# Optimization experiments

Hardware: AMD Instinct MI355X
Metric: run time of the kernel (lower is better)

Reference implementation:

```python
import jax, jax.numpy as jnp
import numpy as np

N0, N1, N2 = 100000, 300000, 150000
P = 2
DIM = 64


def spmm(rows, cols, vals, dense, n_rows):
    # sparse[n_rows, n_cols] @ dense[n_cols, d] via gather + segment_sum
    return jax.ops.segment_sum(vals[:, None] * dense[cols], rows, num_segments=n_rows)


def powcat(X, p):
    # torch.cat([X**1, ..., X**p], dim=1)
    return jnp.concatenate([X ** n for n in range(1, p + 1)], axis=1)


def setup_inputs() -> dict:
    key = jax.random.key(0)
    ks = iter(jax.random.split(key, 64))

    def randn(shape, scale=1.0):
        return jax.random.normal(next(ks), shape, dtype=jnp.float32) * scale

    def sparse(nr, nc, nnz):
        r = jax.random.randint(next(ks), (nnz,), 0, nr, dtype=jnp.int32)
        c = jax.random.randint(next(ks), (nnz,), 0, nc, dtype=jnp.int32)
        v = randn((nnz,), 0.1)
        return r, c, v

    inp = {}
    inp["X0"] = randn((N0, DIM))
    inp["X1"] = randn((N1, DIM))
    inp["X2"] = randn((N2, DIM))
    for name, nr, nc, nnz in [
        ("L0", N0, N0, 1000000),
        ("L1", N1, N1, 2400000),
        ("L2", N2, N2, 1200000),
        ("D1invB1", N0, N1, 600000),
        ("D2B1TD1inv", N1, N0, 600000),
        ("B2TD2inv", N2, N1, 450000),
        ("B2D3", N1, N2, 450000),
    ]:
        r, c, v = sparse(nr, nc, nnz)
        inp[name + "_rows"], inp[name + "_cols"], inp[name + "_vals"] = r, c, v
    wscale = 1.0 / np.sqrt(DIM * P)
    for name in ["n2n", "n2e", "e2e", "e2n", "e2t", "t2e", "t2t"]:
        inp["W_" + name] = randn((DIM * P, DIM), wscale)
        inp["b_" + name] = randn((DIM,), wscale)
    return inp


def reference(X0, X1, X2,
              L0_rows, L0_cols, L0_vals,
              L1_rows, L1_cols, L1_vals,
              L2_rows, L2_cols, L2_vals,
              D1invB1_rows, D1invB1_cols, D1invB1_vals,
              D2B1TD1inv_rows, D2B1TD1inv_cols, D2B1TD1inv_vals,
              B2TD2inv_rows, B2TD2inv_cols, B2TD2inv_vals,
              B2D3_rows, B2D3_cols, B2D3_vals,
              W_n2n, b_n2n, W_n2e, b_n2e, W_e2e, b_e2e, W_e2n, b_e2n,
              W_e2t, b_e2t, W_t2e, b_t2e, W_t2t, b_t2t):
    X0c = powcat(X0, P)  # [N0, 2*d]
    X1c = powcat(X1, P)  # [N1, 2*d]
    X2c = powcat(X2, P)  # [N2, 2*d]

    n2n = spmm(L0_rows, L0_cols, L0_vals, X0c @ W_n2n + b_n2n, N0)
    n2e = spmm(D2B1TD1inv_rows, D2B1TD1inv_cols, D2B1TD1inv_vals, X0c @ W_n2e + b_n2e, N1)
    e2n = spmm(D1invB1_rows, D1invB1_cols, D1invB1_vals, X1c @ W_e2n + b_e2n, N0)
    e2e = spmm(L1_rows, L1_cols, L1_vals, X1c @ W_e2e + b_e2e, N1)
    e2t = spmm(B2TD2inv_rows, B2TD2inv_cols, B2TD2inv_vals, X1c @ W_e2t + b_e2t, N2)
    t2t = spmm(L2_rows, L2_cols, L2_vals, X2c @ W_t2t + b_t2t, N2)
    t2e = spmm(B2D3_rows, B2D3_cols, B2D3_vals, X2c @ W_t2e + b_t2e, N1)

    Y0 = 0.5 * jax.nn.relu(n2n + e2n)
    Y1 = (1.0 / 3.0) * jax.nn.relu(e2e + n2e + t2e)
    Y2 = 0.5 * jax.nn.relu(t2t + e2t)
    return (Y0, Y1, Y2)
```

## Files before the change

### kernel.cpp

```cpp
#include <hip/hip_runtime.h>
#include <hip/hip_bf16.h>


#define RPB 128
#define CAP 2048
#define COL_MASK 0x7FFFFu
#define LROW_SH 19
#define DID_SH 26
#define MAXNB 4352
#define MAXNG 544
#define GRID_BIN 512

typedef __attribute__((ext_vector_type(8))) short short8;
typedef __attribute__((ext_vector_type(4))) float f32x4;

__device__ __forceinline__ int   ntld_i(const int* p)   { return __builtin_nontemporal_load(p); }
__device__ __forceinline__ float ntld_f(const float* p) { return __builtin_nontemporal_load(p); }
__device__ __forceinline__ float4 ntld_f4(const float* p) {
    const unsigned long long* q = (const unsigned long long*)p;
    unsigned long long a = __builtin_nontemporal_load(q);
    unsigned long long b = __builtin_nontemporal_load(q + 1);
    float4 v;
    v.x = __uint_as_float((unsigned)a);
    v.y = __uint_as_float((unsigned)(a >> 32));
    v.z = __uint_as_float((unsigned)b);
    v.w = __uint_as_float((unsigned)(b >> 32));
    return v;
}
__device__ __forceinline__ void ntst_f4(float* p, float4 v) {
    unsigned long long a = (unsigned long long)__float_as_uint(v.x)
                         | ((unsigned long long)__float_as_uint(v.y) << 32);
    unsigned long long b = (unsigned long long)__float_as_uint(v.z)
                         | ((unsigned long long)__float_as_uint(v.w) << 32);
    unsigned long long* q = (unsigned long long*)p;
    __builtin_nontemporal_store(a, q);
    __builtin_nontemporal_store(b, q + 1);
}

__device__ __forceinline__ unsigned short f2bf(float f) {
    unsigned u = __float_as_uint(f);
    unsigned r = u + 0x7FFFu + ((u >> 16) & 1u);
    return (unsigned short)(r >> 16);
}

__device__ __forceinline__ void split8(float4 a0, float4 a1, short8& hi, short8& lo) {
    float v[8] = {a0.x, a0.y, a0.z, a0.w, a1.x, a1.y, a1.z, a1.w};
    #pragma unroll
    for (int e = 0; e < 8; ++e) {
        unsigned short h = f2bf(v[e]);
        float hf = __uint_as_float((unsigned)h << 16);
        hi[e] = (short)h;
        lo[e] = (short)f2bf(v[e] - hf);
    }
}

struct WAll { const float* w[7]; };

__global__ __launch_bounds__(256) void winit(WAll wa, unsigned short* __restrict__ frags)
{
    const int s = blockIdx.x;
    const float* __restrict__ W = wa.w[s];
    unsigned short* __restrict__ out = frags + (size_t)s * 16384;
    for (int slot = threadIdx.x; slot < 1024; slot += 256) {
        const int l  = slot & 63;
        const int nf = (slot >> 6) & 3;
        const int kk = slot >> 8;
        const int col = nf * 16 + (l & 15);
        const int kb  = kk * 32 + 8 * (l >> 4);
        short8 vh, vl;
        #pragma unroll
        for (int e = 0; e < 8; ++e) {
            float w = W[(size_t)(kb + e) * 64 + col];
            unsigned short h = f2bf(w);
            float hf = __uint_as_float((unsigned)h << 16);
            vh[e] = (short)h;
            vl[e] = (short)f2bf(w - hf);
        }
        *(short8*)(out + ((size_t)((kk * 4 + nf) * 2 + 0) * 64 + l) * 8) = vh;
        *(short8*)(out + ((size_t)((kk * 4 + nf) * 2 + 1) * 64 + l) * 8) = vl;
    }
}

__device__ __forceinline__ void mfma_set(
    const short8 Ah[4], const short8 Al[4],
    const unsigned short* __restrict__ F, const float* __restrict__ bias,
    unsigned short* __restrict__ D, int nrows, int row0w, int l)
{
    const int lg = l >> 4, lr = l & 15;
    const short8* __restrict__ Fv = (const short8*)F;
    f32x4 acc[4];
    #pragma unroll
    for (int nf = 0; nf < 4; ++nf) {
        float b = bias[nf * 16 + lr];
        f32x4 bi = {b, b, b, b};
        acc[nf] = bi;
    }
    #pragma unroll
    for (int kk = 0; kk < 4; ++kk) {
        #pragma unroll
        for (int nf = 0; nf < 4; ++nf) {
            short8 bh = Fv[((kk * 4 + nf) * 2 + 0) * 64 + l];
            short8 bl = Fv[((kk * 4 + nf) * 2 + 1) * 64 + l];
            acc[nf] = __builtin_amdgcn_mfma_f32_16x16x32_bf16(Ah[kk], bh, acc[nf], 0, 0, 0);
            acc[nf] = __builtin_amdgcn_mfma_f32_16x16x32_bf16(Al[kk], bh, acc[nf], 0, 0, 0);
            acc[nf] = __builtin_amdgcn_mfma_f32_16x16x32_bf16(Ah[kk], bl, acc[nf], 0, 0, 0);
        }
    }
    #pragma unroll
    for (int nf = 0; nf < 4; ++nf) {
        #pragma unroll
        for (int j = 0; j < 4; ++j) {
            int row = row0w + lg * 4 + j;
            if (row < nrows)
                D[(size_t)row * 64 + nf * 16 + lr] = f2bf(acc[nf][j]);
        }
    }
}

__global__ __launch_bounds__(256) void gemm_powcat_mfma(
    const float* __restrict__ X, int nrows, int nsets,
    const unsigned short* __restrict__ F0, const float* __restrict__ b0, unsigned short* __restrict__ D0,
    const unsigned short* __restrict__ F1, const float* __restrict__ b1, unsigned short* __restrict__ D1,
    const unsigned short* __restrict__ F2, const float* __restrict__ b2, unsigned short* __restrict__ D2)
{
    __shared__ float Xs[64][68];
    const int tid = threadIdx.x;
    const int row0 = blockIdx.x * 64;

    #pragma unroll
    for (int it = 0; it < 4; ++it) {
        int idx = tid + it * 256;
        int r = idx >> 4, c4 = idx & 15;
        float4 v = make_float4(0.f, 0.f, 0.f, 0.f);
        if (row0 + r < nrows)
            v = ntld_f4(X + (size_t)(row0 + r) * 64 + c4 * 4);
        *(float4*)&Xs[r][c4 * 4] = v;
    }
    __syncthreads();

    const int w = tid >> 6, l = tid & 63;
    const int lg = l >> 4, lr = l & 15;

    short8 Ah[4], Al[4];
    #pragma unroll
    for (int kk = 0; kk < 4; ++kk) {
        const float* p = &Xs[w * 16 + lr][(kk & 1) * 32 + 8 * lg];
        float4 a0 = *(const float4*)p;
        float4 a1 = *(const float4*)(p + 4);
        if (kk >= 2) {
            a0.x *= a0.x; a0.y *= a0.y; a0.z *= a0.z; a0.w *= a0.w;
            a1.x *= a1.x; a1.y *= a1.y; a1.z *= a1.z; a1.w *= a1.w;
        }
        split8(a0, a1, Ah[kk], Al[kk]);
    }

    const int row0w = row0 + w * 16;
    mfma_set(Ah, Al, F0, b0, D0, nrows, row0w, l);
    if (nsets > 1) mfma_set(Ah, Al, F1, b1, D1, nrows, row0w, l);
    if (nsets > 2) mfma_set(Ah, Al, F2, b2, D2, nrows, row0w, l);
}

struct Bin7 {
    const int *r0, *r1, *r2, *r3, *r4, *r5, *r6;
    const int *c0, *c1, *c2, *c3, *c4, *c5, *c6;
    const float *v0, *v1, *v2, *v3, *v4, *v5, *v6;
    int p1, p2, p3, p4, p5, p6, p7;
    int t0, t1, t2, t3, t4, t5, t6;
};

struct Ent { int r; int tb; unsigned cw; float v; };

template<bool FULL>
__device__ __forceinline__ Ent decode(const Bin7& B, int i) {
    Ent e;
    if (i < B.p1) {
        int li = i;
        e.r = ntld_i(B.r0 + li); e.tb = B.t0;
        if (FULL) { e.cw = (unsigned)ntld_i(B.c0 + li) | (0u << DID_SH); e.v = ntld_f(B.v0 + li); }
    } else if (i < B.p2) {
        int li = i - B.p1;
        e.r = ntld_i(B.r1 + li); e.tb = B.t1;
        if (FULL) { e.cw = (unsigned)ntld_i(B.c1 + li) | (1u << DID_SH); e.v = ntld_f(B.v1 + li); }
    } else if (i < B.p3) {
        int li = i - B.p2;
        e.r = ntld_i(B.r2 + li); e.tb = B.t2;
        if (FULL) { e.cw = (unsigned)ntld_i(B.c2 + li) | (2u << DID_SH); e.v = ntld_f(B.v2 + li); }
    } else if (i < B.p4) {
        int li = i - B.p3;
        e.r = ntld_i(B.r3 + li); e.tb = B.t3;
        if (FULL) { e.cw = (unsigned)ntld_i(B.c3 + li) | (3u << DID_SH); e.v = ntld_f(B.v3 + li); }
    } else if (i < B.p5) {
        int li = i - B.p4;
        e.r = ntld_i(B.r4 + li); e.tb = B.t4;
        if (FULL) { e.cw = (unsigned)ntld_i(B.c4 + li) | (4u << DID_SH); e.v = ntld_f(B.v4 + li); }
    } else if (i < B.p6) {
        int li = i - B.p5;
        e.r = ntld_i(B.r5 + li); e.tb = B.t5;
        if (FULL) { e.cw = (unsigned)ntld_i(B.c5 + li) | (5u << DID_SH); e.v = ntld_f(B.v5 + li); }
    } else {
        int li = i - B.p6;
        e.r = ntld_i(B.r6 + li); e.tb = B.t6;
        if (FULL) { e.cw = (unsigned)ntld_i(B.c6 + li) | (6u << DID_SH); e.v = ntld_f(B.v6 + li); }
    }
    return e;
}

__global__ __launch_bounds__(1024) void bhist_grp(
    Bin7 B, int* __restrict__ gcount, int NG, int chunk)
{
    __shared__ int h[MAXNG];
    for (int i = threadIdx.x; i < NG; i += 1024) h[i] = 0;
    __syncthreads();
    const int s = blockIdx.x * chunk;
    int e = s + chunk;  if (e > B.p7) e = B.p7;
    for (int i = s + threadIdx.x; i < e; i += 1024) {
        Ent en = decode<false>(B, i);
        atomicAdd(&h[(en.tb + (en.r >> 7)) >> 3], 1);
    }
    __syncthreads();
    for (int i = threadIdx.x; i < NG; i += 1024)
        if (h[i]) atomicAdd(&gcount[i], h[i]);
}

__global__ __launch_bounds__(1024) void scatter_grp(
    Bin7 B, int* __restrict__ gcur, uint2* __restrict__ payA,
    int NG, int chunk)
{
    __shared__ int lbase[MAXNG];
    __shared__ int lcur[MAXNG];
    for (int i = threadIdx.x; i < NG; i += 1024) lcur[i] = 0;
    __syncthreads();
    const int s = blockIdx.x * chunk;
    int e = s + chunk;  if (e > B.p7) e = B.p7;

    for (int i = s + threadIdx.x; i < e; i += 1024) {
        Ent en = decode<false>(B, i);
        atomicAdd(&lcur[(en.tb + (en.r >> 7)) >> 3], 1);
    }
    __syncthreads();
    for (int i = threadIdx.x; i < NG; i += 1024) {
        int c = lcur[i];
        lbase[i] = c ? atomicAdd(&gcur[i], c) : 0;
        lcur[i] = 0;
    }
    __syncthreads();
    for (int i = s + threadIdx.x; i < e; i += 1024) {
        Ent en = decode<true>(B, i);
        int b = en.tb + (en.r >> 7);
        int g = b >> 3;
        int pos = lbase[g] + atomicAdd(&lcur[g], 1);
        unsigned col = en.cw & COL_MASK;
        unsigned did = en.cw >> DID_SH;
        unsigned cwA = col | ((unsigned)(en.r & 127) << LROW_SH)
                     | ((unsigned)(b & 7) << 26) | (did << 29);
        payA[pos] = make_uint2(cwA, __float_as_uint(en.v));
    }
}

__global__ __launch_bounds__(1024) void sort_grp(
    const uint2* __restrict__ payA, const int* __restrict__ goff,
    const int* __restrict__ gcur, int* __restrict__ boff,
    int* __restrict__ bend, uint2* __restrict__ payB, int NBtot)
{
    __shared__ int cnt[8], cur[8];
    const int g = blockIdx.x;
    const int b0 = g * 8;
    const int seg0 = goff[g], seg1 = gcur[g];
    if (threadIdx.x < 8) cnt[threadIdx.x] = 0;
    __syncthreads();
    for (int i = seg0 + threadIdx.x; i < seg1; i += 1024) {
        unsigned w = __builtin_nontemporal_load(&payA[i].x);
        atomicAdd(&cnt[(w >> 26) & 7], 1);
    }
    __syncthreads();
    if (threadIdx.x == 0) {
        int base = seg0;
        #pragma unroll
        for (int j = 0; j < 8; ++j) {
            cur[j] = base;
            if (b0 + j < NBtot) { boff[b0 + j] = base; bend[b0 + j] = base + cnt[j]; }
            base += cnt[j];
        }
    }
    __syncthreads();
    for (int i = seg0 + threadIdx.x; i < seg1; i += 1024) {
        unsigned long long pv = __builtin_nontemporal_load(
            (const unsigned long long*)(payA + i));
        unsigned w = (unsigned)pv;
        int j = (w >> 26) & 7;
        int pos = atomicAdd(&cur[j], 1);
        unsigned cw = (w & 0x03FFFFFFu) | ((w >> 29) << 26);
        payB[pos] = make_uint2(cw, (unsigned)(pv >> 32));
    }
}

__global__ __launch_bounds__(1024) void scan_small(
    const int* __restrict__ in, int* __restrict__ boff,
    int* __restrict__ bcur, int n)
{
    __shared__ int wsum[16];
    __shared__ int carry;
    const int tid = threadIdx.x, lane = tid & 63, wv = tid >> 6;
    if (tid == 0) carry = 0;
    __syncthreads();
    for (int base = 0; base < n; base += 4096) {
        int i = base + tid * 4;
        int v0 = (i + 0 < n) ? in[i + 0] : 0;
        int v1 = (i + 1 < n) ? in[i + 1] : 0;
        int v2 = (i + 2 < n) ? in[i + 2] : 0;
        int v3 = (i + 3 < n) ? in[i + 3] : 0;
        int tsum = v0 + v1 + v2 + v3;
        int x = tsum;
        #pragma unroll
        for (int off = 1; off < 64; off <<= 1) {
            int y = __shfl_up(x, off);
            if (lane >= off) x += y;
        }
        if (lane == 63) wsum[wv] = x;
        int c0 = carry;
        __syncthreads();
        if (tid < 16) {
            int ss = wsum[tid];
            #pragma unroll
            for (int off = 1; off < 16; off <<= 1) {
                int y = __shfl_up(ss, off, 16);
                if (tid >= off) ss += y;
            }
            wsum[tid] = ss;
        }
        __syncthreads();
        int wpre = (wv == 0) ? 0 : wsum[wv - 1];
        int excl = c0 + wpre + (x - tsum);
        if (i + 0 < n) { boff[i + 0] = excl; bcur[i + 0] = excl; } excl += v0;
        if (i + 1 < n) { boff[i + 1] = excl; bcur[i + 1] = excl; } excl += v1;
        if (i + 2 < n) { boff[i + 2] = excl; bcur[i + 2] = excl; } excl += v2;
        if (i + 3 < n) { boff[i + 3] = excl; bcur[i + 3] = excl; }
        __syncthreads();
        if (tid == 0) carry = c0 + wsum[15];
        __syncthreads();
    }
}

__global__ __launch_bounds__(256) void spmm_fused7(
    const uint2* __restrict__ bpay, const int* __restrict__ boff,
    const int* __restrict__ bend,
    const unsigned short* __restrict__ d0, const unsigned short* __restrict__ d1,
    const unsigned short* __restrict__ d2, const unsigned short* __restrict__ d3,
    const unsigned short* __restrict__ d4, const unsigned short* __restrict__ d5,
    const unsigned short* __restrict__ d6,
    float* __restrict__ out, int tile0, int nrows,
    int firstWrite, int doRelu, float scale, int didMask)
{
    __shared__ uint2 pay[CAP];
    __shared__ unsigned short sidx[CAP];
    __shared__ int lcount[128], loff[128], lcur[128];
    __shared__ int s_w0;
    __shared__ const unsigned short* dptr[8];

    const int tid = threadIdx.x;
    const int t = tile0 + blockIdx.x;

    if (tid == 0) {
        dptr[0] = d0; dptr[1] = d1; dptr[2] = d2; dptr[3] = d3;
        dptr[4] = d4; dptr[5] = d5; dptr[6] = d6; dptr[7] = d0;
    }
    __syncthreads();

    const int seg0  = boff[t];
    const int total = bend[t] - seg0;
    const int nchunks = (total + CAP - 1) / CAP;
    const int qw = tid >> 4, l = tid & 15;
    const int row0 = blockIdx.x * RPB;

    float4 acc[8];
    #pragma unroll
    for (int rr = 0; rr < 8; ++rr) acc[rr] = make_float4(0.f, 0.f, 0.f, 0.f);

    for (int c = 0; c < nchunks; ++c) {
        if (tid < 128) lcount[tid] = 0;
        __syncthreads();

        const int cbase = c * CAP;
        int ccnt = total - cbase;
        if (ccnt > CAP) ccnt = CAP;

        for (int i = tid; i < ccnt; i += 256) {
            unsigned long long pv = __builtin_nontemporal_load(
                (const unsigned long long*)(bpay + seg0 + cbase + i));
            uint2 p = make_uint2((unsigned)pv, (unsigned)(pv >> 32));
            pay[i] = p;
            atomicAdd(&lcount[(p.x >> LROW_SH) & 127], 1);
        }
        __syncthreads();

        int xv = 0;
        if (tid < 128) xv = lcount[tid];
        #pragma unroll
        for (int off = 1; off < 64; off <<= 1) {
            int y = __shfl_up(xv, off);
            if ((tid & 63) >= off) xv += y;
        }
        if (tid == 63) s_w0 = xv;
        __syncthreads();
        if (tid < 128) {
            int incl = xv + ((tid >= 64) ? s_w0 : 0);
            loff[tid] = incl - lcount[tid];
            lcur[tid] = incl - lcount[tid];
        }
        __syncthreads();

        for (int i = tid; i < ccnt; i += 256) {
            int lr = (pay[i].x >> LROW_SH) & 127;
            int pos = atomicAdd(&lcur[lr], 1);
            sidx[pos] = (unsigned short)i;
        }
        __syncthreads();

        #pragma unroll
        for (int rr = 0; rr < 8; ++rr) {
            int lr = rr * 16 + qw;
            int ss = loff[lr], ee = ss + lcount[lr];
            float4 a = acc[rr];
            for (int j = ss; j < ee; ++j) {
                uint2 p = pay[sidx[j]];
                int did = (int)(p.x >> DID_SH) & 7;
                if (!((didMask >> did) & 1)) continue;
                int col = p.x & COL_MASK;
                float v = __uint_as_float(p.y);
                const uint2* Dg = reinterpret_cast<const uint2*>(dptr[did]);
                uint2 d = Dg[(size_t)col * 16 + l];
                a.x = fmaf(v, __uint_as_float((d.x & 0xFFFFu) << 16), a.x);
                a.y = fmaf(v, __uint_as_float(d.x & 0xFFFF0000u), a.y);
                a.z = fmaf(v, __uint_as_float((d.y & 0xFFFFu) << 16), a.z);
                a.w = fmaf(v, __uint_as_float(d.y & 0xFFFF0000u), a.w);
            }
            acc[rr] = a;
        }
        __syncthreads();
    }

    #pragma unroll
    for (int rr = 0; rr < 8; ++rr) {
        int lr = rr * 16 + qw;
        int row = row0 + lr;
        if (row < nrows) {
            float* o = out + (size_t)row * 64 + l * 4;
            float4 a = acc[rr];
            if (!firstWrite) {
                float4 cur = *reinterpret_cast<float4*>(o);
                a.x += cur.x; a.y += cur.y; a.z += cur.z; a.w += cur.w;
            }
            if (doRelu) {
                a.x = fmaxf(a.x, 0.f) * scale;
                a.y = fmaxf(a.y, 0.f) * scale;
                a.z = fmaxf(a.z, 0.f) * scale;
                a.w = fmaxf(a.w, 0.f) * scale;
            }
            ntst_f4(o, a);
        }
    }
}

extern "C" void kernel_launch(void* const* d_in, const int* in_sizes, int n_in,
                              void* d_out, int out_size, void* d_ws, size_t ws_size,
                              hipStream_t stream)
{
    const float* X0 = (const float*)d_in[0];
    const float* X1 = (const float*)d_in[1];
    const float* X2 = (const float*)d_in[2];
    const int N0 = in_sizes[0] / 64;
    const int N1 = in_sizes[1] / 64;
    const int N2 = in_sizes[2] / 64;

    auto Wp = [&](int i) { return (const float*)d_in[24 + 2 * i]; };
    auto bp = [&](int i) { return (const float*)d_in[25 + 2 * i]; };
    auto Sr = [&](int i) { return (const int*)d_in[3 + 3 * i]; };
    auto Sc = [&](int i) { return (const int*)d_in[4 + 3 * i]; };
    auto Sv = [&](int i) { return (const float*)d_in[5 + 3 * i]; };
    auto Sn = [&](int i) { return in_sizes[3 + 3 * i]; };

    const size_t offY1 = (size_t)N0 * 64;
    const size_t offY2 = (size_t)(N0 + N1) * 64;
    const float TH = 1.0f / 3.0f;

    const int NB0 = (N0 + RPB - 1) / RPB;
    const int NB1 = (N1 + RPB - 1) / RPB;
    const int NB2 = (N2 + RPB - 1) / RPB;

    float* out = (float*)d_out;
    auto align256 = [](size_t x) { return (x + 255) & ~(size_t)255; };

    const size_t FRAG_SET = 16384;
    const size_t fragB = align256(7 * FRAG_SET * sizeof(unsigned short));
    if (ws_size <= fragB) return;
    unsigned short* wfrags = (unsigned short*)d_ws;
    char* ws = (char*)d_ws + fragB;
    const size_t ws_avail = ws_size - fragB;
    auto wf = [&](int i) { return wfrags + (size_t)i * FRAG_SET; };

    WAll wa;
    for (int i = 0; i < 7; ++i) wa.w[i] = Wp(i);
    winit<<<7, 256, 0, stream>>>(wa, wfrags);

    const int NBall = NB0 + NB1 + NB2;
    const int NGall = (NBall + 7) / 8;
    const int nnzAll = Sn(0)+Sn(1)+Sn(2)+Sn(3)+Sn(4)+Sn(5)+Sn(6);
    const size_t payAsz = (size_t)nnzAll * sizeof(uint2);
    const size_t payT1 = align256(payAsz);
    const size_t cntT1 = align256((size_t)(NBall + 8) * sizeof(int));
    const size_t denseT1 = ((size_t)2*N0 + 3*N1 + 2*N2) * 64 * sizeof(unsigned short);
    const size_t regionT1 = denseT1 > payT1 ? denseT1 : payT1;
    const size_t needT1 = payT1 + 5 * cntT1 + regionT1;

    if (ws_avail >= needT1 && NBall <= MAXNB) {
        uint2* payB  = (uint2*)ws;
        int* goff    = (int*)(ws + payT1);
        int* gcur    = (int*)(ws + payT1 + 1 * cntT1);
        int* boff    = (int*)(ws + payT1 + 2 * cntT1);
        int* bend    = (int*)(ws + payT1 + 3 * cntT1);
        int* gcount  = (int*)(ws + payT1 + 4 * cntT1);
        char* region = ws + payT1 + 5 * cntT1;
        uint2* payA  = (uint2*)region;
        unsigned short* db = (unsigned short*)region;
        unsigned short* dn2n = db;
        unsigned short* de2n = dn2n + (size_t)N0 * 64;
        unsigned short* dn2e = de2n + (size_t)N1 * 64;
        unsigned short* de2e = dn2e + (size_t)N0 * 64;
        unsigned short* dt2e = de2e + (size_t)N1 * 64;
        unsigned short* de2t = dt2e + (size_t)N2 * 64;
        unsigned short* dt2t = de2t + (size_t)N1 * 64;

        Bin7 B;
        B.r0 = Sr(0); B.c0 = Sc(0); B.v0 = Sv(0);
        B.r1 = Sr(3); B.c1 = Sc(3); B.v1 = Sv(3);
        B.r2 = Sr(4); B.c2 = Sc(4); B.v2 = Sv(4);
        B.r3 = Sr(1); B.c3 = Sc(1); B.v3 = Sv(1);
        B.r4 = Sr(6); B.c4 = Sc(6); B.v4 = Sv(6);
        B.r5 = Sr(5); B.c5 = Sc(5); B.v5 = Sv(5);
        B.r6 = Sr(2); B.c6 = Sc(2); B.v6 = Sv(2);
        B.p1 = Sn(0);
        B.p2 = B.p1 + Sn(3);
        B.p3 = B.p2 + Sn(4);
        B.p4 = B.p3 + Sn(1);
        B.p5 = B.p4 + Sn(6);
        B.p6 = B.p5 + Sn(5);
        B.p7 = B.p6 + Sn(2);
        B.t0 = 0;   B.t1 = 0;
        B.t2 = NB0; B.t3 = NB0; B.t4 = NB0;
        B.t5 = NB0 + NB1; B.t6 = NB0 + NB1;

        const int chunk = (B.p7 + GRID_BIN - 1) / GRID_BIN;
        hipMemsetAsync(gcount, 0, (size_t)NGall * sizeof(int), stream);
        bhist_grp<<<GRID_BIN, 1024, 0, stream>>>(B, gcount, NGall, chunk);
        scan_small<<<1, 1024, 0, stream>>>(gcount, goff, gcur, NGall);
        scatter_grp<<<GRID_BIN, 1024, 0, stream>>>(B, gcur, payA, NGall, chunk);
        sort_grp<<<NGall, 1024, 0, stream>>>(payA, goff, gcur, boff, bend, payB, NBall);

        gemm_powcat_mfma<<<(N0 + 63) / 64, 256, 0, stream>>>(
            X0, N0, 2,
            wf(0), bp(0), dn2n,
            wf(1), bp(1), dn2e,
            wf(0), bp(0), dn2n);
        gemm_powcat_mfma<<<(N1 + 63) / 64, 256, 0, stream>>>(
            X1, N1, 3,
            wf(3), bp(3), de2n,
            wf(2), bp(2), de2e,
            wf(4), bp(4), de2t);
        gemm_powcat_mfma<<<(N2 + 63) / 64, 256, 0, stream>>>(
            X2, N2, 2,
            wf(5), bp(5), dt2e,
            wf(6), bp(6), dt2t,
            wf(5), bp(5), dt2e);

        spmm_fused7<<<NB0, 256, 0, stream>>>(payB, boff, bend,
            dn2n, de2n, dn2e, de2e, dt2e, de2t, dt2t,
            out, 0, N0, 1, 1, 0.5f, 0x7F);
        spmm_fused7<<<NB1, 256, 0, stream>>>(payB, boff, bend,
            dn2n, de2n, dn2e, de2e, dt2e, de2t, dt2t,
            out + offY1, NB0, N1, 1, 1, TH, 0x7F);
        spmm_fused7<<<NB2, 256, 0, stream>>>(payB, boff, bend,
            dn2n, de2n, dn2e, de2e, dt2e, de2t, dt2t,
            out + offY2, NB0 + NB1, N2, 1, 1, 0.5f, 0x7F);
        return;
    }

    const int NBtotA = NB0 + NB2;
    const int NBmax = NBtotA > NB1 ? NBtotA : NB1;
    const int nnzA = Sn(0) + Sn(3) + Sn(5) + Sn(2);
    const int nnzB = Sn(4) + Sn(6) + Sn(1);
    const int nnzMax = nnzA > nnzB ? nnzA : nnzB;

    const size_t payBsz = align256((size_t)nnzMax * sizeof(uint2));
    const size_t cntB = align256((size_t)(NBmax + 8) * sizeof(int));
    const size_t denseOff = payBsz + 5 * cntB;

    uint2* bpayB = (uint2*)ws;
    int* goff    = (int*)(ws + payBsz);
    int* gcur    = (int*)(ws + payBsz + 1 * cntB);
    int* boff    = (int*)(ws + payBsz + 2 * cntB);
    int* bend    = (int*)(ws + payBsz + 3 * cntB);
    int* gcount  = (int*)(ws + payBsz + 4 * cntB);
    unsigned short* dense = (unsigned short*)(ws + denseOff);
    uint2* payA  = (uint2*)dense;

    const size_t need_full = denseOff +
        ((size_t)N0 + N2 + N1) * 64 * sizeof(unsigned short);
    const bool fullB = (ws_avail >= need_full);

    {
        Bin7 B;
        B.r0 = Sr(0); B.c0 = Sc(0); B.v0 = Sv(0);
        B.r1 = Sr(3); B.c1 = Sc(3); B.v1 = Sv(3);
        B.r2 = Sr(5); B.c2 = Sc(5); B.v2 = Sv(5);
        B.r3 = Sr(2); B.c3 = Sc(2); B.v3 = Sv(2);
        B.r4 = B.r3; B.c4 = B.c3; B.v4 = B.v3;
        B.r5 = B.r3; B.c5 = B.c3; B.v5 = B.v3;
        B.r6 = B.r3; B.c6 = B.c3; B.v6 = B.v3;
        B.p1 = Sn(0);
        B.p2 = B.p1 + Sn(3);
        B.p3 = B.p2 + Sn(5);
        B.p4 = B.p3 + Sn(2);
        B.p5 = B.p4; B.p6 = B.p4; B.p7 = B.p4;
        B.t0 = 0; B.t1 = 0; B.t2 = NB0; B.t3 = NB0;
        B.t4 = NB0; B.t5 = NB0; B.t6 = NB0;

        const int NGA = (NBtotA + 7) / 8;
        const int chunk = (B.p7 + GRID_BIN - 1) / GRID_BIN;
        hipMemsetAsync(gcount, 0, (size_t)NGA * sizeof(int), stream);
        bhist_grp<<<GRID_BIN, 1024, 0, stream>>>(B, gcount, NGA, chunk);
        scan_small<<<1, 1024, 0, stream>>>(gcount, goff, gcur, NGA);
        scatter_grp<<<GRID_BIN, 1024, 0, stream>>>(B, gcur, payA, NGA, chunk);
        sort_grp<<<NGA, 1024, 0, stream>>>(payA, goff, gcur, boff, bend, bpayB, NBtotA);

        unsigned short* dn2n = dense;
        unsigned short* de2n = dense + (size_t)N0 * 64;
        gemm_powcat_mfma<<<(N0 + 63) / 64, 256, 0, stream>>>(
            X0, N0, 1, wf(0), bp(0), dn2n,
            wf(0), bp(0), dn2n, wf(0), bp(0), dn2n);
        gemm_powcat_mfma<<<(N1 + 63) / 64, 256, 0, stream>>>(
            X1, N1, 1, wf(3), bp(3), de2n,
            wf(3), bp(3), de2n, wf(3), bp(3), de2n);
        spmm_fused7<<<NB0, 256, 0, stream>>>(bpayB, boff, bend,
            dn2n, de2n, dn2n, dn2n, dn2n, dn2n, dn2n,
            out, 0, N0, 1, 1, 0.5f, 0x7F);

        unsigned short* de2t = dense;
        unsigned short* dt2t = dense + (size_t)N1 * 64;
        gemm_powcat_mfma<<<(N1 + 63) / 64, 256, 0, stream>>>(
            X1, N1, 1, wf(4), bp(4), de2t,
            wf(4), bp(4), de2t, wf(4), bp(4), de2t);
        gemm_powcat_mfma<<<(N2 + 63) / 64, 256, 0, stream>>>(
            X2, N2, 1, wf(6), bp(6), dt2t,
            wf(6), bp(6), dt2t, wf(6), bp(6), dt2t);
        spmm_fused7<<<NB2, 256, 0, stream>>>(bpayB, boff, bend,
            de2t, de2t, de2t, dt2t, de2t, de2t, de2t,
            out + offY2, NB0, N2, 1, 1, 0.5f, 0x7F);
    }

    {
        Bin7 B;
        B.r0 = Sr(4); B.c0 = Sc(4); B.v0 = Sv(4);
        B.r1 = Sr(6); B.c1 = Sc(6); B.v1 = Sv(6);
        B.r2 = Sr(1); B.c2 = Sc(1); B.v2 = Sv(1);
        B.r3 = B.r2; B.c3 = B.c2; B.v3 = B.v2;
        B.r4 = B.r2; B.c4 = B.c2; B.v4 = B.v2;
        B.r5 = B.r2; B.c5 = B.c2; B.v5 = B.v2;
        B.r6 = B.r2; B.c6 = B.c2; B.v6 = B.v2;
        B.p1 = Sn(4);
        B.p2 = B.p1 + Sn(6);
        B.p3 = B.p2 + Sn(1);
        B.p4 = B.p3; B.p5 = B.p3; B.p6 = B.p3; B.p7 = B.p3;
        B.t0 = 0; B.t1 = 0; B.t2 = 0; B.t3 = 0; B.t4 = 0; B.t5 = 0; B.t6 = 0;

        const int NGB = (NB1 + 7) / 8;
        const int chunk = (B.p7 + GRID_BIN - 1) / GRID_BIN;
        hipMemsetAsync(gcount, 0, (size_t)NGB * sizeof(int), stream);
        bhist_grp<<<GRID_BIN, 1024, 0, stream>>>(B, gcount, NGB, chunk);
        scan_small<<<1, 1024, 0, stream>>>(gcount, goff, gcur, NGB);
        scatter_grp<<<GRID_BIN, 1024, 0, stream>>>(B, gcur, payA, NGB, chunk);
        sort_grp<<<NGB, 1024, 0, stream>>>(payA, goff, gcur, boff, bend, bpayB, NB1);

        if (fullB) {
            unsigned short* dn2e = dense;
            unsigned short* dt2e = dense + (size_t)N0 * 64;
            unsigned short* de2e = dense + ((size_t)N0 + N2) * 64;
            gemm_powcat_mfma<<<(N0 + 63) / 64, 256, 0, stream>>>(
                X0, N0, 1, wf(1), bp(1), dn2e,
                wf(1), bp(1), dn2e, wf(1), bp(1), dn2e);
            gemm_powcat_mfma<<<(N2 + 63) / 64, 256, 0, stream>>>(
                X2, N2, 1, wf(5), bp(5), dt2e,
                wf(5), bp(5), dt2e, wf(5), bp(5), dt2e);
            gemm_powcat_mfma<<<(N1 + 63) / 64, 256, 0, stream>>>(
                X1, N1, 1, wf(2), bp(2), de2e,
                wf(2), bp(2), de2e, wf(2), bp(2), de2e);
            spmm_fused7<<<NB1, 256, 0, stream>>>(bpayB, boff, bend,
                dn2e, dt2e, de2e, dn2e, dn2e, dn2e, dn2e,
                out + offY1, 0, N1, 1, 1, TH, 0x7F);
        } else {
            unsigned short* dn2e = dense;
            unsigned short* dt2e = dense + (size_t)N0 * 64;
            gemm_powcat_mfma<<<(N0 + 63) / 64, 256, 0, stream>>>(
                X0, N0, 1, wf(1), bp(1), dn2e,
                wf(1), bp(1), dn2e, wf(1), bp(1), dn2e);
            gemm_powcat_mfma<<<(N2 + 63) / 64, 256, 0, stream>>>(
                X2, N2, 1, wf(5), bp(5), dt2e,
                wf(5), bp(5), dt2e, wf(5), bp(5), dt2e);
            spmm_fused7<<<NB1, 256, 0, stream>>>(bpayB, boff, bend,
                dn2e, dt2e, dn2e, dn2e, dn2e, dn2e, dn2e,
                out + offY1, 0, N1, 1, 0, 0.f, 0x3);
            unsigned short* de2e = dense;
            gemm_powcat_mfma<<<(N1 + 63) / 64, 256, 0, stream>>>(
                X1, N1, 1, wf(2), bp(2), de2e,
                wf(2), bp(2), de2e, wf(2), bp(2), de2e);
            spmm_fused7<<<NB1, 256, 0, stream>>>(bpayB, boff, bend,
                de2e, de2e, de2e, de2e, de2e, de2e, de2e,
                out + offY1, 0, N1, 0, 1, TH, 0x4);
        }
    }
}
```

Measured before the change: 598.1 us.

## Sort payload fully by row in sort_grp and stream CSR rows in SpMM

The group sort now bins entries into 1024 per-row buckets (8 tiles by 128 local rows) instead of 8 tile buckets, and writes a per-row offset array. The SpMM kernel no longer stages chunks in LDS, counts, scans and index-sorts per tile. It reads each row's contiguous range straight from global memory, with software prefetch of the next payload and dense row. This removes LDS traffic and several block barriers from the SpMM. In exchange, sort_grp does more shared-memory atomics and a block-wide scan, and a row-offset array is added to the workspace.

```diff
diff --git a/kernel.cpp b/kernel.cpp
--- a/kernel.cpp
+++ b/kernel.cpp
@@ -3,7 +3,6 @@
 
 
 #define RPB 128
-#define CAP 2048
 #define COL_MASK 0x7FFFFu
 #define LROW_SH 19
 #define DID_SH 26
@@ -259,36 +258,57 @@
 
 __global__ __launch_bounds__(1024) void sort_grp(
     const uint2* __restrict__ payA, const int* __restrict__ goff,
-    const int* __restrict__ gcur, int* __restrict__ boff,
+    const int* __restrict__ gcur, int* __restrict__ rowoff,
     int* __restrict__ bend, uint2* __restrict__ payB, int NBtot)
 {
-    __shared__ int cnt[8], cur[8];
+    __shared__ int cnt[1024];
+    __shared__ int cur[1024];
+    __shared__ int wsum[16];
     const int g = blockIdx.x;
-    const int b0 = g * 8;
+    const int tid = threadIdx.x;
     const int seg0 = goff[g], seg1 = gcur[g];
-    if (threadIdx.x < 8) cnt[threadIdx.x] = 0;
-    __syncthreads();
-    for (int i = seg0 + threadIdx.x; i < seg1; i += 1024) {
+
+    cnt[tid] = 0;
+    __syncthreads();
+    for (int i = seg0 + tid; i < seg1; i += 1024) {
         unsigned w = __builtin_nontemporal_load(&payA[i].x);
-        atomicAdd(&cnt[(w >> 26) & 7], 1);
-    }
-    __syncthreads();
-    if (threadIdx.x == 0) {
-        int base = seg0;
+        atomicAdd(&cnt[(w >> 19) & 1023], 1);
+    }
+    __syncthreads();
+
+    const int lane = tid & 63, wv = tid >> 6;
+    int tot = cnt[tid];
+    int x = tot;
+    #pragma unroll
+    for (int off = 1; off < 64; off <<= 1) {
+        int y = __shfl_up(x, off);
+        if (lane >= off) x += y;
+    }
+    if (lane == 63) wsum[wv] = x;
+    __syncthreads();
+    if (tid < 16) {
+        int ss = wsum[tid];
         #pragma unroll
-        for (int j = 0; j < 8; ++j) {
-            cur[j] = base;
-            if (b0 + j < NBtot) { boff[b0 + j] = base; bend[b0 + j] = base + cnt[j]; }
-            base += cnt[j];
-        }
-    }
-    __syncthreads();
-    for (int i = seg0 + threadIdx.x; i < seg1; i += 1024) {
+        for (int off = 1; off < 16; off <<= 1) {
+            int y = __shfl_up(ss, off, 16);
+            if (tid >= off) ss += y;
+        }
+        wsum[tid] = ss;
+    }
+    __syncthreads();
+    int pos0 = seg0 + (x - tot) + ((wv == 0) ? 0 : wsum[wv - 1]);
+    cur[tid] = pos0;
+    rowoff[(size_t)g * 1024 + tid] = pos0;
+    int b = g * 8 + (tid >> 7);
+    if (b < NBtot && (tid & 127) == 127) bend[b] = pos0 + tot;
+    __syncthreads();
+
+    for (int i = seg0 + tid; i < seg1; i += 1024) {
         unsigned long long pv = __builtin_nontemporal_load(
             (const unsigned long long*)(payA + i));
         unsigned w = (unsigned)pv;
-        int j = (w >> 26) & 7;
-        int pos = atomicAdd(&cur[j], 1);
+        int bin = (w >> 19) & 1023;
+        int pos = atomicAdd(&cur[bin], 1);
         unsigned cw = (w & 0x03FFFFFFu) | ((w >> 29) << 26);
         payB[pos] = make_uint2(cw, (unsigned)(pv >> 32));
     }
@@ -341,8 +361,8 @@
     }
 }
 
-__global__ __launch_bounds__(256) void spmm_fused7(
-    const uint2* __restrict__ bpay, const int* __restrict__ boff,
+__global__ __launch_bounds__(256) void spmm_stream7(
+    const uint2* __restrict__ payB, const int* __restrict__ rowoff,
     const int* __restrict__ bend,
     const unsigned short* __restrict__ d0, const unsigned short* __restrict__ d1,
     const unsigned short* __restrict__ d2, const unsigned short* __restrict__ d3,
@@ -351,101 +371,55 @@
     float* __restrict__ out, int tile0, int nrows,
     int firstWrite, int doRelu, float scale, int didMask)
 {
-    __shared__ uint2 pay[CAP];
-    __shared__ unsigned short sidx[CAP];
-    __shared__ int lcount[128], loff[128], lcur[128];
-    __shared__ int s_w0;
     __shared__ const unsigned short* dptr[8];
-
     const int tid = threadIdx.x;
+    if (tid < 8) {
+        const unsigned short* tbl[8] = {d0, d1, d2, d3, d4, d5, d6, d0};
+        dptr[tid] = tbl[tid];
+    }
+    __syncthreads();
+
     const int t = tile0 + blockIdx.x;
-
-    if (tid == 0) {
-        dptr[0] = d0; dptr[1] = d1; dptr[2] = d2; dptr[3] = d3;
-        dptr[4] = d4; dptr[5] = d5; dptr[6] = d6; dptr[7] = d0;
-    }
-    __syncthreads();
-
-    const int seg0  = boff[t];
-    const int total = bend[t] - seg0;
-    const int nchunks = (total + CAP - 1) / CAP;
     const int qw = tid >> 4, l = tid & 15;
     const int row0 = blockIdx.x * RPB;
-
-    float4 acc[8];
-    #pragma unroll
-    for (int rr = 0; rr < 8; ++rr) acc[rr] = make_float4(0.f, 0.f, 0.f, 0.f);
-
-    for (int c = 0; c < nchunks; ++c) {
-        if (tid < 128) lcount[tid] = 0;
-        __syncthreads();
-
-        const int cbase = c * CAP;
-        int ccnt = total - cbase;
-        if (ccnt > CAP) ccnt = CAP;
-
-        for (int i = tid; i < ccnt; i += 256) {
-            unsigned long long pv = __builtin_nontemporal_load(
-                (const unsigned long long*)(bpay + seg0 + cbase + i));
-            uint2 p = make_uint2((unsigned)pv, (unsigned)(pv >> 32));
-            pay[i] = p;
-            atomicAdd(&lcount[(p.x >> LROW_SH) & 127], 1);
-        }
-        __syncthreads();
-
-        int xv = 0;
-        if (tid < 128) xv = lcount[tid];
-        #pragma unroll
-        for (int off = 1; off < 64; off <<= 1) {
-            int y = __shfl_up(xv, off);
-            if ((tid & 63) >= off) xv += y;
-        }
-        if (tid == 63) s_w0 = xv;
-        __syncthreads();
-        if (tid < 128) {
-            int incl = xv + ((tid >= 64) ? s_w0 : 0);
-            loff[tid] = incl - lcount[tid];
-            lcur[tid] = incl - lcount[tid];
-        }
-        __syncthreads();
-
-        for (int i = tid; i < ccnt; i += 256) {
-            int lr = (pay[i].x >> LROW_SH) & 127;
-            int pos = atomicAdd(&lcur[lr], 1);
-            sidx[pos] = (unsigned short)i;
-        }
-        __syncthreads();
-
-        #pragma unroll
-        for (int rr = 0; rr < 8; ++rr) {
-            int lr = rr * 16 + qw;
-            int ss = loff[lr], ee = ss + lcount[lr];
-            float4 a = acc[rr];
-            for (int j = ss; j < ee; ++j) {
-                uint2 p = pay[sidx[j]];
-                int did = (int)(p.x >> DID_SH) & 7;
-                if (!((didMask >> did) & 1)) continue;
-                int col = p.x & COL_MASK;
-                float v = __uint_as_float(p.y);
-                const uint2* Dg = reinterpret_cast<const uint2*>(dptr[did]);
-                uint2 d = Dg[(size_t)col * 16 + l];
-                a.x = fmaf(v, __uint_as_float((d.x & 0xFFFFu) << 16), a.x);
-                a.y = fmaf(v, __uint_as_float(d.x & 0xFFFF0000u), a.y);
-                a.z = fmaf(v, __uint_as_float((d.y & 0xFFFFu) << 16), a.z);
-                a.w = fmaf(v, __uint_as_float(d.y & 0xFFFF0000u), a.w);
+    const int rbase = t * RPB;
+    const int bendt = bend[t];
+
+    #pragma unroll 1
+    for (int rr = 0; rr < 8; ++rr) {
+        const int lr = rr * 16 + qw;
+        const int row = row0 + lr;
+        const int js = rowoff[rbase + lr];
+        const int je = (lr == 127) ? bendt : rowoff[rbase + lr + 1];
+        float4 a = make_float4(0.f, 0.f, 0.f, 0.f);
+
+        if (js < je) {
+            const int jlast = je - 1;
+            uint2 pA = payB[js];
+            uint2 pB = payB[js < jlast ? js + 1 : jlast];
+            const uint2* DgA = reinterpret_cast<const uint2*>(dptr[(pA.x >> DID_SH) & 7]);
+            uint2 dA = DgA[(size_t)(pA.x & COL_MASK) * 16 + l];
+            float vA = ((didMask >> ((pA.x >> DID_SH) & 7)) & 1) ? __uint_as_float(pA.y) : 0.f;
+
+            for (int j = js; j < je; ++j) {
+                uint2 dcur = dA;
+                float vcur = vA;
+                uint2 pN = pB;
+                int j2 = j + 2 <= jlast ? j + 2 : jlast;
+                pB = payB[j2];
+                const uint2* Dg = reinterpret_cast<const uint2*>(dptr[(pN.x >> DID_SH) & 7]);
+                dA = Dg[(size_t)(pN.x & COL_MASK) * 16 + l];
+                vA = ((didMask >> ((pN.x >> DID_SH) & 7)) & 1) ? __uint_as_float(pN.y) : 0.f;
+
+                a.x = fmaf(vcur, __uint_as_float((dcur.x & 0xFFFFu) << 16), a.x);
+                a.y = fmaf(vcur, __uint_as_float(dcur.x & 0xFFFF0000u), a.y);
+                a.z = fmaf(vcur, __uint_as_float((dcur.y & 0xFFFFu) << 16), a.z);
+                a.w = fmaf(vcur, __uint_as_float(dcur.y & 0xFFFF0000u), a.w);
             }
-            acc[rr] = a;
-        }
-        __syncthreads();
-    }
-
-    #pragma unroll
-    for (int rr = 0; rr < 8; ++rr) {
-        int lr = rr * 16 + qw;
-        int row = row0 + lr;
+        }
+
         if (row < nrows) {
             float* o = out + (size_t)row * 64 + l * 4;
-            float4 a = acc[rr];
             if (!firstWrite) {
                 float4 cur = *reinterpret_cast<float4*>(o);
                 a.x += cur.x; a.y += cur.y; a.z += cur.z; a.w += cur.w;
@@ -505,21 +479,21 @@
     const int NBall = NB0 + NB1 + NB2;
     const int NGall = (NBall + 7) / 8;
     const int nnzAll = Sn(0)+Sn(1)+Sn(2)+Sn(3)+Sn(4)+Sn(5)+Sn(6);
-    const size_t payAsz = (size_t)nnzAll * sizeof(uint2);
-    const size_t payT1 = align256(payAsz);
+    const size_t payT1 = align256((size_t)nnzAll * sizeof(uint2));
     const size_t cntT1 = align256((size_t)(NBall + 8) * sizeof(int));
+    const size_t rowT1 = align256((size_t)NGall * 1024 * sizeof(int));
     const size_t denseT1 = ((size_t)2*N0 + 3*N1 + 2*N2) * 64 * sizeof(unsigned short);
     const size_t regionT1 = denseT1 > payT1 ? denseT1 : payT1;
-    const size_t needT1 = payT1 + 5 * cntT1 + regionT1;
+    const size_t needT1 = payT1 + 4 * cntT1 + rowT1 + regionT1;
 
     if (ws_avail >= needT1 && NBall <= MAXNB) {
         uint2* payB  = (uint2*)ws;
         int* goff    = (int*)(ws + payT1);
         int* gcur    = (int*)(ws + payT1 + 1 * cntT1);
-        int* boff    = (int*)(ws + payT1 + 2 * cntT1);
-        int* bend    = (int*)(ws + payT1 + 3 * cntT1);
-        int* gcount  = (int*)(ws + payT1 + 4 * cntT1);
-        char* region = ws + payT1 + 5 * cntT1;
+        int* bend    = (int*)(ws + payT1 + 2 * cntT1);
+        int* gcount  = (int*)(ws + payT1 + 3 * cntT1);
+        int* rowoff  = (int*)(ws + payT1 + 4 * cntT1);
+        char* region = ws + payT1 + 4 * cntT1 + rowT1;
         uint2* payA  = (uint2*)region;
         unsigned short* db = (unsigned short*)region;
         unsigned short* dn2n = db;
@@ -554,7 +528,7 @@
         bhist_grp<<<GRID_BIN, 1024, 0, stream>>>(B, gcount, NGall, chunk);
         scan_small<<<1, 1024, 0, stream>>>(gcount, goff, gcur, NGall);
         scatter_grp<<<GRID_BIN, 1024, 0, stream>>>(B, gcur, payA, NGall, chunk);
-        sort_grp<<<NGall, 1024, 0, stream>>>(payA, goff, gcur, boff, bend, payB, NBall);
+        sort_grp<<<NGall, 1024, 0, stream>>>(payA, goff, gcur, rowoff, bend, payB, NBall);
 
         gemm_powcat_mfma<<<(N0 + 63) / 64, 256, 0, stream>>>(
             X0, N0, 2,
@@ -572,13 +546,13 @@
             wf(6), bp(6), dt2t,
             wf(5), bp(5), dt2e);
 
-        spmm_fused7<<<NB0, 256, 0, stream>>>(payB, boff, bend,
+        spmm_stream7<<<NB0, 256, 0, stream>>>(payB, rowoff, bend,
             dn2n, de2n, dn2e, de2e, dt2e, de2t, dt2t,
             out, 0, N0, 1, 1, 0.5f, 0x7F);
-        spmm_fused7<<<NB1, 256, 0, stream>>>(payB, boff, bend,
+        spmm_stream7<<<NB1, 256, 0, stream>>>(payB, rowoff, bend,
             dn2n, de2n, dn2e, de2e, dt2e, de2t, dt2t,
             out + offY1, NB0, N1, 1, 1, TH, 0x7F);
-        spmm_fused7<<<NB2, 256, 0, stream>>>(payB, boff, bend,
+        spmm_stream7<<<NB2, 256, 0, stream>>>(payB, rowoff, bend,
             dn2n, de2n, dn2e, de2e, dt2e, de2t, dt2t,
             out + offY2, NB0 + NB1, N2, 1, 1, 0.5f, 0x7F);
         return;
@@ -586,20 +560,22 @@
 
     const int NBtotA = NB0 + NB2;
     const int NBmax = NBtotA > NB1 ? NBtotA : NB1;
+    const int NGmax = (NBmax + 7) / 8;
     const int nnzA = Sn(0) + Sn(3) + Sn(5) + Sn(2);
     const int nnzB = Sn(4) + Sn(6) + Sn(1);
     const int nnzMax = nnzA > nnzB ? nnzA : nnzB;
 
     const size_t payBsz = align256((size_t)nnzMax * sizeof(uint2));
     const size_t cntB = align256((size_t)(NBmax + 8) * sizeof(int));
-    const size_t denseOff = payBsz + 5 * cntB;
+    const size_t rowB = align256((size_t)NGmax * 1024 * sizeof(int));
+    const size_t denseOff = payBsz + 4 * cntB + rowB;
 
     uint2* bpayB = (uint2*)ws;
     int* goff    = (int*)(ws + payBsz);
     int* gcur    = (int*)(ws + payBsz + 1 * cntB);
-    int* boff    = (int*)(ws + payBsz + 2 * cntB);
-    int* bend    = (int*)(ws + payBsz + 3 * cntB);
-    int* gcount  = (int*)(ws + payBsz + 4 * cntB);
+    int* bend    = (int*)(ws + payBsz + 2 * cntB);
+    int* gcount  = (int*)(ws + payBsz + 3 * cntB);
+    int* rowoff  = (int*)(ws + payBsz + 4 * cntB);
     unsigned short* dense = (unsigned short*)(ws + denseOff);
     uint2* payA  = (uint2*)dense;
 
@@ -630,7 +606,7 @@
         bhist_grp<<<GRID_BIN, 1024, 0, stream>>>(B, gcount, NGA, chunk);
         scan_small<<<1, 1024, 0, stream>>>(gcount, goff, gcur, NGA);
         scatter_grp<<<GRID_BIN, 1024, 0, stream>>>(B, gcur, payA, NGA, chunk);
-        sort_grp<<<NGA, 1024, 0, stream>>>(payA, goff, gcur, boff, bend, bpayB, NBtotA);
+        sort_grp<<<NGA, 1024, 0, stream>>>(payA, goff, gcur, rowoff, bend, bpayB, NBtotA);
 
         unsigned short* dn2n = dense;
         unsigned short* de2n = dense + (size_t)N0 * 64;
@@ -640,7 +616,7 @@
         gemm_powcat_mfma<<<(N1 + 63) / 64, 256, 0, stream>>>(
             X1, N1, 1, wf(3), bp(3), de2n,
             wf(3), bp(3), de2n, wf(3), bp(3), de2n);
-        spmm_fused7<<<NB0, 256, 0, stream>>>(bpayB, boff, bend,
+        spmm_stream7<<<NB0, 256, 0, stream>>>(bpayB, rowoff, bend,
             dn2n, de2n, dn2n, dn2n, dn2n, dn2n, dn2n,
             out, 0, N0, 1, 1, 0.5f, 0x7F);
 
@@ -652,7 +628,7 @@
         gemm_powcat_mfma<<<(N2 + 63) / 64, 256, 0, stream>>>(
             X2, N2, 1, wf(6), bp(6), dt2t,
             wf(6), bp(6), dt2t, wf(6), bp(6), dt2t);
-        spmm_fused7<<<NB2, 256, 0, stream>>>(bpayB, boff, bend,
+        spmm_stream7<<<NB2, 256, 0, stream>>>(bpayB, rowoff, bend,
             de2t, de2t, de2t, dt2t, de2t, de2t, de2t,
             out + offY2, NB0, N2, 1, 1, 0.5f, 0x7F);
     }
@@ -678,7 +654,7 @@
         bhist_grp<<<GRID_BIN, 1024, 0, stream>>>(B, gcount, NGB, chunk);
         scan_small<<<1, 1024, 0, stream>>>(gcount, goff, gcur, NGB);
         scatter_grp<<<GRID_BIN, 1024, 0, stream>>>(B, gcur, payA, NGB, chunk);
-        sort_grp<<<NGB, 1024, 0, stream>>>(payA, goff, gcur, boff, bend, bpayB, NB1);
+        sort_grp<<<NGB, 1024, 0, stream>>>(payA, goff, gcur, rowoff, bend, bpayB, NB1);
 
         if (fullB) {
             unsigned short* dn2e = dense;
@@ -693,7 +669,7 @@
             gemm_powcat_mfma<<<(N1 + 63) / 64, 256, 0, stream>>>(
                 X1, N1, 1, wf(2), bp(2), de2e,
                 wf(2), bp(2), de2e, wf(2), bp(2), de2e);
-            spmm_fused7<<<NB1, 256, 0, stream>>>(bpayB, boff, bend,
+            spmm_stream7<<<NB1, 256, 0, stream>>>(bpayB, rowoff, bend,
                 dn2e, dt2e, de2e, dn2e, dn2e, dn2e, dn2e,
                 out + offY1, 0, N1, 1, 1, TH, 0x7F);
         } else {
@@ -705,14 +681,14 @@
             gemm_powcat_mfma<<<(N2 + 63) / 64, 256, 0, stream>>>(
                 X2, N2, 1, wf(5), bp(5), dt2e,
                 wf(5), bp(5), dt2e, wf(5), bp(5), dt2e);
-            spmm_fused7<<<NB1, 256, 0, stream>>>(bpayB, boff, bend,
+            spmm_stream7<<<NB1, 256, 0, stream>>>(bpayB, rowoff, bend,
                 dn2e, dt2e, dn2e, dn2e, dn2e, dn2e, dn2e,
                 out + offY1, 0, N1, 1, 0, 0.f, 0x3);
             unsigned short* de2e = dense;
             gemm_powcat_mfma<<<(N1 + 63) / 64, 256, 0, stream>>>(
                 X1, N1, 1, wf(2), bp(2), de2e,
                 wf(2), bp(2), de2e, wf(2), bp(2), de2e);
-            spmm_fused7<<<NB1, 256, 0, stream>>>(bpayB, boff, bend,
+            spmm_stream7<<<NB1, 256, 0, stream>>>(bpayB, rowoff, bend,
                 de2e, de2e, de2e, de2e, de2e, de2e, de2e,
                 out + offY1, 0, N1, 0, 1, TH, 0x4);
         }
```

New measurement: 651.2 us. 8.9% more time.
